# Performance work log

Measured on AMD Instinct MI355X. Metric: run time of the kernel, lower is better.

The kernel has to match this reference:

```python
import jax, jax.numpy as jnp
import numpy as np

N = 50000      # nodes
C = 64         # in_channels
O = 64         # out_channels (== in_channels, required by zeros_like in original)
S = 8          # size: number of weight matrices
E = 1700000    # edges (neighbor pairs incl. self-loops), avg degree ~34


def setup_inputs() -> dict:
    key = jax.random.key(0)
    ks = jax.random.split(key, 9)
    node_tensor = jax.random.normal(ks[0], (N, C), dtype=jnp.float32)
    src = jax.random.randint(ks[1], (E,), 0, N)                 # neighbor node j
    dst = jnp.sort(jax.random.randint(ks[2], (E,), 0, N))       # center node i
    sc = 1.0 / np.sqrt(C)
    W = jax.random.normal(ks[3], (S, C, O), dtype=jnp.float32) * sc   # linears weights
    b = jax.random.normal(ks[4], (S, O), dtype=jnp.float32) * sc      # linears biases
    Ws = jax.random.normal(ks[5], (C, S), dtype=jnp.float32) * sc     # source proj
    bs = jax.random.normal(ks[6], (S,), dtype=jnp.float32) * sc
    Wt = jax.random.normal(ks[7], (C, S), dtype=jnp.float32) * sc     # target proj
    bt = jax.random.normal(ks[8], (S,), dtype=jnp.float32) * sc
    return dict(node_tensor=node_tensor, src=src, dst=dst,
                W=W, b=b, Ws=Ws, bs=bs, Wt=Wt, bt=bt)


def reference(node_tensor, src, dst, W, b, Ws, bs, Wt, bt):
    # Per-node soft-assignment logits (FeaStNet)
    s = node_tensor @ Ws + bs          # [N, S] : source_tensor
    t = node_tensor @ Wt + bt          # [N, S] : target_tensor
    # Per-edge assignment: softmax over the `size` dim of source[center] + target[neighbor]
    q = jax.nn.softmax(s[dst] + t[src], axis=-1)      # [E, S]
    # Per-matrix projected node features: weighted[m] = x @ W_m + b_m
    Wx = jnp.einsum('nc,sco->sno', node_tensor, W) + b[:, None, :]   # [S, N, O]
    # msg[e] = sum_m q[e,m] * Wx[m, src[e]]; loop over small fixed S to avoid [S,E,O] blowup
    msg = q[:, 0:1] * Wx[0][src]                      # [E, O]
    for m in range(1, S):
        msg = msg + q[:, m:m + 1] * Wx[m][src]
    # Scatter-sum over each center's neighborhood, mean over the S weight matrices
    out = jax.ops.segment_sum(msg, dst, num_segments=N) / S          # [N, O]
    return out
```

## Files before the change

### kernel.cpp

```cpp
#include <hip/hip_runtime.h>
#include <hip/hip_bf16.h>


#define CDIM 64
#define SDIM 8

typedef __bf16 bf16x8 __attribute__((ext_vector_type(8)));
typedef float f32x4 __attribute__((ext_vector_type(4)));

__global__ __launch_bounds__(256) void k1_pre(
    const float* __restrict__ x, const float* __restrict__ Ws,
    const float* __restrict__ bs, const float* __restrict__ Wt,
    const float* __restrict__ bt, const float* __restrict__ W,
    const int* __restrict__ dst, float* __restrict__ ST,
    __hip_bfloat16* __restrict__ xbf, __hip_bfloat16* __restrict__ WtB,
    int* __restrict__ rowptr, int N, int E, int nbN) {
  int bid = blockIdx.x;
  if (bid >= nbN + 128) {
    int e = (bid - nbN - 128) * 256 + threadIdx.x;
    if (e >= E) return;
    int a = dst[e];
    int bnd = (e + 1 < E) ? dst[e + 1] : N;
    if (e == 0) {
      for (int d = 0; d <= a; ++d) rowptr[d] = 0;
    }
    for (int d = a + 1; d <= bnd; ++d) rowptr[d] = e + 1;
    return;
  }
  if (bid >= nbN) {
    int t = (bid - nbN) * 256 + threadIdx.x;
    int o = t >> 9, k = t & 511;
    WtB[t] = __float2bfloat16(W[(size_t)k * 64 + o]);
    return;
  }

  __shared__ __hip_bfloat16 wst[16 * 72];
  __shared__ float bst[16];
  int t = threadIdx.x;
#pragma unroll
  for (int j = 0; j < 4; ++j) {
    int idx = t * 4 + j;
    int n = idx >> 6, k = idx & 63;
    float v = (n < 8) ? Ws[k * 8 + n] : Wt[k * 8 + (n - 8)];
    wst[n * 72 + k] = __float2bfloat16(v);
  }
  if (t < 16) bst[t] = (t < 8) ? bs[t] : bt[t - 8];
  __syncthreads();

  int wave = t >> 6, lane = t & 63;
  int r = lane & 15, q = lane >> 4;
  int node = bid * 64 + wave * 16 + r;
  int nodec = node < N ? node : N - 1;
  const float* xr = x + (size_t)nodec * CDIM;

  bf16x8 afrag[2];
#pragma unroll
  for (int kt = 0; kt < 2; ++kt) {
    float4 u0 = *(const float4*)(xr + kt * 32 + q * 8);
    float4 u1 = *(const float4*)(xr + kt * 32 + q * 8 + 4);
    union { bf16x8 v; __hip_bfloat16 h[8]; } a;
    a.h[0] = __float2bfloat16(u0.x); a.h[1] = __float2bfloat16(u0.y);
    a.h[2] = __float2bfloat16(u0.z); a.h[3] = __float2bfloat16(u0.w);
    a.h[4] = __float2bfloat16(u1.x); a.h[5] = __float2bfloat16(u1.y);
    a.h[6] = __float2bfloat16(u1.z); a.h[7] = __float2bfloat16(u1.w);
    afrag[kt] = a.v;
    if (node < N)
      *(bf16x8*)(xbf + (size_t)node * CDIM + kt * 32 + q * 8) = a.v;
  }

  bf16x8 bf0 = *(const bf16x8*)(wst + r * 72 + q * 8);
  bf16x8 bf1 = *(const bf16x8*)(wst + r * 72 + 32 + q * 8);

  f32x4 acc = {0, 0, 0, 0};
  acc = __builtin_amdgcn_mfma_f32_16x16x32_bf16(afrag[0], bf0, acc, 0, 0, 0);
  acc = __builtin_amdgcn_mfma_f32_16x16x32_bf16(afrag[1], bf1, acc, 0, 0, 0);

  int m = lane & 15;
#pragma unroll
  for (int v = 0; v < 4; ++v) {
    int nd = bid * 64 + wave * 16 + q * 4 + v;
    if (nd >= N) continue;
    float val = acc[v] + bst[m];
    if (m >= 8) val = __expf(val);
    ST[nd * 16 + m] = val;
  }
}

__global__ __launch_bounds__(256) void k3_mfma(
    const __hip_bfloat16* __restrict__ xbf, const int* __restrict__ src,
    const int* __restrict__ rowptr, const float* __restrict__ ST,
    __hip_bfloat16* __restrict__ Gbf, float* __restrict__ R, int N) {
  __shared__ __hip_bfloat16 qt_s[4][16 * 40];
  __shared__ __hip_bfloat16 xt_s[4][32 * 72];

  int wave = threadIdx.x >> 6;
  int lane = threadIdx.x & 63;
  int i = blockIdx.x * 4 + wave;
  if (i >= N) return;

  int mm = lane & 7;
  int kk = lane >> 3;
  int mp = lane & 15;
  int q3 = lane >> 4;

  __hip_bfloat16* qt = &qt_s[wave][0];
  __hip_bfloat16* xt = &xt_s[wave][0];

  __hip_bfloat16 z0 = __float2bfloat16(0.0f);
#pragma unroll
  for (int z = 0; z < 5; ++z) qt[320 + z * 64 + lane] = z0;

  int lo = rowptr[i];
  int hi = rowptr[i + 1];
  float uv = __expf(ST[i * 16 + mm]);

  f32x4 acc0 = {0, 0, 0, 0}, acc1 = {0, 0, 0, 0};
  f32x4 acc2 = {0, 0, 0, 0}, acc3 = {0, 0, 0, 0};
  float racc = 0.f;

  if (lo < hi) {
    int ecl = hi - 1;
    int iv[4];
#pragma unroll
    for (int g = 0; g < 4; ++g) {
      int ek = lo + g * 8 + kk;
      iv[g] = src[ek < ecl ? ek : ecl];
    }

    for (int c0 = lo; c0 < hi; c0 += 32) {
      bf16x8 xv[4];
#pragma unroll
      for (int g = 0; g < 4; ++g)
        xv[g] = *(const bf16x8*)(xbf + (size_t)iv[g] * CDIM + mm * 8);

      float tv[4];
#pragma unroll
      for (int g = 0; g < 4; ++g) tv[g] = ST[iv[g] * 16 + 8 + mm];

      int nc0 = c0 + 32;
      int niv[4];
#pragma unroll
      for (int g = 0; g < 4; ++g) {
        int ek = nc0 + g * 8 + kk;
        ek = ek < ecl ? ek : ecl;
        niv[g] = (nc0 < hi) ? src[ek] : iv[g];
      }

#pragma unroll
      for (int g = 0; g < 4; ++g) {
        float w = uv * tv[g];
        float ssum = w + __shfl_xor(w, 1);
        ssum += __shfl_xor(ssum, 2);
        ssum += __shfl_xor(ssum, 4);
        float qv = w * __frcp_rn(ssum);
        if (c0 + g * 8 + kk >= hi) qv = 0.f;
        racc += qv;
        qt[mm * 40 + g * 8 + kk] = __float2bfloat16(qv);
      }

#pragma unroll
      for (int g = 0; g < 4; ++g)
        *(bf16x8*)(xt + (g * 8 + kk) * 72 + mm * 8) = xv[g];

      bf16x8 afrag = *(const bf16x8*)(qt + mp * 40 + q3 * 8);

      {
        union { bf16x8 v; __hip_bfloat16 h[8]; } b0, b1, b2, b3;
#pragma unroll
        for (int j = 0; j < 8; ++j) {
          const __hip_bfloat16* xr = xt + (q3 * 8 + j) * 72 + mp;
          b0.h[j] = xr[0];
          b1.h[j] = xr[16];
          b2.h[j] = xr[32];
          b3.h[j] = xr[48];
        }
        acc0 = __builtin_amdgcn_mfma_f32_16x16x32_bf16(afrag, b0.v, acc0, 0, 0, 0);
        acc1 = __builtin_amdgcn_mfma_f32_16x16x32_bf16(afrag, b1.v, acc1, 0, 0, 0);
        acc2 = __builtin_amdgcn_mfma_f32_16x16x32_bf16(afrag, b2.v, acc2, 0, 0, 0);
        acc3 = __builtin_amdgcn_mfma_f32_16x16x32_bf16(afrag, b3.v, acc3, 0, 0, 0);
      }

      iv[0] = niv[0]; iv[1] = niv[1]; iv[2] = niv[2]; iv[3] = niv[3];
    }
  }

  if (q3 < 2) {
    __hip_bfloat16* Gi = Gbf + (size_t)i * 512;
#pragma unroll
    for (int v = 0; v < 4; ++v) {
      int m = q3 * 4 + v;
      Gi[m * 64 + 0 + mp]  = __float2bfloat16(acc0[v]);
      Gi[m * 64 + 16 + mp] = __float2bfloat16(acc1[v]);
      Gi[m * 64 + 32 + mp] = __float2bfloat16(acc2[v]);
      Gi[m * 64 + 48 + mp] = __float2bfloat16(acc3[v]);
    }
  }

  racc += __shfl_xor(racc, 8);
  racc += __shfl_xor(racc, 16);
  racc += __shfl_xor(racc, 32);
  if (lane < 8) R[(size_t)i * 8 + lane] = racc;
}

__global__ __launch_bounds__(256) void k4_mfma(
    const __hip_bfloat16* __restrict__ Gbf, const float* __restrict__ R,
    const __hip_bfloat16* __restrict__ WtB, const float* __restrict__ bias,
    float* __restrict__ out, int N) {
  __shared__ float4 btile[64 * 65];
  {
    const float4* srcp = (const float4*)WtB;
    int t = threadIdx.x;
#pragma unroll
    for (int j = 0; j < 16; ++j) {
      int ci = t + j * 256;
      btile[(ci >> 6) * 65 + (ci & 63)] = srcp[ci];
    }
  }
  __syncthreads();

  int wave = threadIdx.x >> 6;
  int lane = threadIdx.x & 63;
  int r0 = (blockIdx.x * 4 + wave) * 16;
  if (r0 >= N) return;

  int m = lane & 15;
  int q = lane >> 4;
  const __bf16* abase = (const __bf16*)(Gbf + (size_t)(r0 + m) * 512) + q * 8;
  const __bf16* lbase = (const __bf16*)btile + (size_t)m * 520 + q * 8;

  f32x4 acc0 = {0, 0, 0, 0}, acc1 = {0, 0, 0, 0};
  f32x4 acc2 = {0, 0, 0, 0}, acc3 = {0, 0, 0, 0};
#pragma unroll
  for (int kt = 0; kt < 16; ++kt) {
    bf16x8 a = *(const bf16x8*)(abase + kt * 32);
    bf16x8 b0 = *(const bf16x8*)(lbase + 0 * 520 + kt * 32);
    bf16x8 b1 = *(const bf16x8*)(lbase + 16 * 520 + kt * 32);
    bf16x8 b2 = *(const bf16x8*)(lbase + 32 * 520 + kt * 32);
    bf16x8 b3 = *(const bf16x8*)(lbase + 48 * 520 + kt * 32);
    acc0 = __builtin_amdgcn_mfma_f32_16x16x32_bf16(a, b0, acc0, 0, 0, 0);
    acc1 = __builtin_amdgcn_mfma_f32_16x16x32_bf16(a, b1, acc1, 0, 0, 0);
    acc2 = __builtin_amdgcn_mfma_f32_16x16x32_bf16(a, b2, acc2, 0, 0, 0);
    acc3 = __builtin_amdgcn_mfma_f32_16x16x32_bf16(a, b3, acc3, 0, 0, 0);
  }

#pragma unroll
  for (int v = 0; v < 4; ++v) {
    int ri = r0 + q * 4 + v;
    if (ri >= N) continue;
    const float* Ri = R + (size_t)ri * 8;
    float b0s = 0, b1s = 0, b2s = 0, b3s = 0;
#pragma unroll
    for (int mm = 0; mm < 8; ++mm) {
      float rv = Ri[mm];
      b0s = fmaf(rv, bias[mm * 64 + 0 + m], b0s);
      b1s = fmaf(rv, bias[mm * 64 + 16 + m], b1s);
      b2s = fmaf(rv, bias[mm * 64 + 32 + m], b2s);
      b3s = fmaf(rv, bias[mm * 64 + 48 + m], b3s);
    }
    float* orow = out + (size_t)ri * 64;
    orow[0 + m]  = (acc0[v] + b0s) * 0.125f;
    orow[16 + m] = (acc1[v] + b1s) * 0.125f;
    orow[32 + m] = (acc2[v] + b2s) * 0.125f;
    orow[48 + m] = (acc3[v] + b3s) * 0.125f;
  }
}

extern "C" void kernel_launch(void* const* d_in, const int* in_sizes, int n_in,
                              void* d_out, int out_size, void* d_ws, size_t ws_size,
                              hipStream_t stream) {
  const float* x  = (const float*)d_in[0];
  const int* src  = (const int*)d_in[1];
  const int* dst  = (const int*)d_in[2];
  const float* W  = (const float*)d_in[3];
  const float* b  = (const float*)d_in[4];
  const float* Ws = (const float*)d_in[5];
  const float* bs = (const float*)d_in[6];
  const float* Wt = (const float*)d_in[7];
  const float* bt = (const float*)d_in[8];
  int N = in_sizes[0] / CDIM;
  int E = in_sizes[1];
  float* out = (float*)d_out;

  float* ST = (float*)d_ws;
  __hip_bfloat16* Gbf = (__hip_bfloat16*)(ST + (size_t)N * 16);
  float* R  = (float*)(Gbf + (size_t)N * 512);
  __hip_bfloat16* WtB = (__hip_bfloat16*)(R + (size_t)N * 8);
  __hip_bfloat16* xbf = WtB + 64 * 512;
  int* rowptr = (int*)(xbf + (size_t)N * CDIM);

  int nbN = (N + 63) / 64;
  int nbE = (E + 255) / 256;
  k1_pre<<<nbN + 128 + nbE, 256, 0, stream>>>(x, Ws, bs, Wt, bt, W, dst, ST,
                                              xbf, WtB, rowptr, N, E, nbN);
  k3_mfma<<<(N + 3) / 4, 256, 0, stream>>>(xbf, src, rowptr, ST, Gbf, R, N);
  int mtiles = (N + 15) / 16;
  k4_mfma<<<(mtiles + 3) / 4, 256, 0, stream>>>(Gbf, R, WtB, b, out, N);
}
```

Baseline: 158.3 us.

## Software-pipeline neighbor gathers, use LDS transpose reads, drop k4 weight staging

In the per-node aggregation kernel, the gathers of neighbor features and target logits are now issued one chunk ahead (double buffering), with the source indices prefetched two chunks ahead, so the gather latency can overlap the softmax and MFMA work. The scalar strided LDS reads that built the B fragments are replaced by ds_read_b64_tr_b16 transpose loads over a new 16-wide tiled LDS layout. Launch bounds now request occupancy 4. The final GEMM kernel reads the bf16 weights directly from global memory (cache) instead of staging them in padded LDS with a block barrier. The costs are higher register pressure from the prefetch buffers, inline asm with an explicit full lgkmcnt wait, and weight loads that are no longer served from LDS.

Result: slower. 182.5 us (+15.3%).

```diff
diff --git a/kernel.cpp b/kernel.cpp
--- a/kernel.cpp
+++ b/kernel.cpp
@@ -6,6 +6,7 @@
 #define SDIM 8
 
 typedef __bf16 bf16x8 __attribute__((ext_vector_type(8)));
+typedef __bf16 bf16x4 __attribute__((ext_vector_type(4)));
 typedef float f32x4 __attribute__((ext_vector_type(4)));
 
 __global__ __launch_bounds__(256) void k1_pre(
@@ -86,12 +87,12 @@
   }
 }
 
-__global__ __launch_bounds__(256) void k3_mfma(
+__global__ __launch_bounds__(256, 4) void k3_mfma(
     const __hip_bfloat16* __restrict__ xbf, const int* __restrict__ src,
     const int* __restrict__ rowptr, const float* __restrict__ ST,
     __hip_bfloat16* __restrict__ Gbf, float* __restrict__ R, int N) {
   __shared__ __hip_bfloat16 qt_s[4][16 * 40];
-  __shared__ __hip_bfloat16 xt_s[4][32 * 72];
+  __shared__ __hip_bfloat16 xt_s[4][4 * 32 * 16];
 
   int wave = threadIdx.x >> 6;
   int lane = threadIdx.x & 63;
@@ -114,36 +115,56 @@
   int hi = rowptr[i + 1];
   float uv = __expf(ST[i * 16 + mm]);
 
+  unsigned rd_addr = (unsigned)(uintptr_t)xt + (unsigned)q3 * 256u +
+                     (unsigned)mp * 8u;
+  __hip_bfloat16* xw = xt + (mm >> 1) * 512 + (mm & 1) * 8;
+
   f32x4 acc0 = {0, 0, 0, 0}, acc1 = {0, 0, 0, 0};
   f32x4 acc2 = {0, 0, 0, 0}, acc3 = {0, 0, 0, 0};
   float racc = 0.f;
 
   if (lo < hi) {
     int ecl = hi - 1;
-    int iv[4];
+    int iv[4], niv[4];
+    bf16x8 xv[4];
+    float tv[4];
+
 #pragma unroll
     for (int g = 0; g < 4; ++g) {
       int ek = lo + g * 8 + kk;
       iv[g] = src[ek < ecl ? ek : ecl];
     }
+#pragma unroll
+    for (int g = 0; g < 4; ++g)
+      xv[g] = *(const bf16x8*)(xbf + (size_t)iv[g] * CDIM + mm * 8);
+#pragma unroll
+    for (int g = 0; g < 4; ++g) tv[g] = ST[iv[g] * 16 + 8 + mm];
+    if (lo + 32 < hi) {
+#pragma unroll
+      for (int g = 0; g < 4; ++g) {
+        int ek = lo + 32 + g * 8 + kk;
+        niv[g] = src[ek < ecl ? ek : ecl];
+      }
+    }
 
     for (int c0 = lo; c0 < hi; c0 += 32) {
-      bf16x8 xv[4];
-#pragma unroll
-      for (int g = 0; g < 4; ++g)
-        xv[g] = *(const bf16x8*)(xbf + (size_t)iv[g] * CDIM + mm * 8);
-
-      float tv[4];
-#pragma unroll
-      for (int g = 0; g < 4; ++g) tv[g] = ST[iv[g] * 16 + 8 + mm];
-
-      int nc0 = c0 + 32;
-      int niv[4];
-#pragma unroll
-      for (int g = 0; g < 4; ++g) {
-        int ek = nc0 + g * 8 + kk;
-        ek = ek < ecl ? ek : ecl;
-        niv[g] = (nc0 < hi) ? src[ek] : iv[g];
+      bool hasn = (c0 + 32 < hi);
+      bf16x8 nxv[4];
+      float ntv[4];
+      int nniv[4];
+      if (hasn) {
+#pragma unroll
+        for (int g = 0; g < 4; ++g)
+          nxv[g] = *(const bf16x8*)(xbf + (size_t)niv[g] * CDIM + mm * 8);
+#pragma unroll
+        for (int g = 0; g < 4; ++g) ntv[g] = ST[niv[g] * 16 + 8 + mm];
+        if (c0 + 64 < hi) {
+#pragma unroll
+          for (int g = 0; g < 4; ++g) {
+            int ek = c0 + 64 + g * 8 + kk;
+            nniv[g] = src[ek < ecl ? ek : ecl];
+          }
+        }
       }
 
 #pragma unroll
@@ -160,27 +181,47 @@
 
 #pragma unroll
       for (int g = 0; g < 4; ++g)
-        *(bf16x8*)(xt + (g * 8 + kk) * 72 + mm * 8) = xv[g];
+        *(bf16x8*)(xw + (g * 8 + kk) * 16) = xv[g];
 
       bf16x8 afrag = *(const bf16x8*)(qt + mp * 40 + q3 * 8);
 
-      {
-        union { bf16x8 v; __hip_bfloat16 h[8]; } b0, b1, b2, b3;
-#pragma unroll
-        for (int j = 0; j < 8; ++j) {
-          const __hip_bfloat16* xr = xt + (q3 * 8 + j) * 72 + mp;
-          b0.h[j] = xr[0];
-          b1.h[j] = xr[16];
-          b2.h[j] = xr[32];
-          b3.h[j] = xr[48];
+      bf16x4 t0, t1, t2, t3, t4, t5, t6, t7;
+      asm volatile(
+          "ds_read_b64_tr_b16 %0, %8 offset:0\n\t"
+          "ds_read_b64_tr_b16 %1, %8 offset:128\n\t"
+          "ds_read_b64_tr_b16 %2, %8 offset:1024\n\t"
+          "ds_read_b64_tr_b16 %3, %8 offset:1152\n\t"
+          "ds_read_b64_tr_b16 %4, %8 offset:2048\n\t"
+          "ds_read_b64_tr_b16 %5, %8 offset:2176\n\t"
+          "ds_read_b64_tr_b16 %6, %8 offset:3072\n\t"
+          "ds_read_b64_tr_b16 %7, %8 offset:3200"
+          : "=&v"(t0), "=&v"(t1), "=&v"(t2), "=&v"(t3),
+            "=&v"(t4), "=&v"(t5), "=&v"(t6), "=&v"(t7)
+          : "v"(rd_addr)
+          : "memory");
+      asm volatile("s_waitcnt lgkmcnt(0)" ::: "memory");
+      __builtin_amdgcn_sched_barrier(0);
+
+      union { bf16x8 v; bf16x4 h[2]; } b0, b1, b2, b3;
+      b0.h[0] = t0; b0.h[1] = t1;
+      b1.h[0] = t2; b1.h[1] = t3;
+      b2.h[0] = t4; b2.h[1] = t5;
+      b3.h[0] = t6; b3.h[1] = t7;
+
+      acc0 = __builtin_amdgcn_mfma_f32_16x16x32_bf16(afrag, b0.v, acc0, 0, 0, 0);
+      acc1 = __builtin_amdgcn_mfma_f32_16x16x32_bf16(afrag, b1.v, acc1, 0, 0, 0);
+      acc2 = __builtin_amdgcn_mfma_f32_16x16x32_bf16(afrag, b2.v, acc2, 0, 0, 0);
+      acc3 = __builtin_amdgcn_mfma_f32_16x16x32_bf16(afrag, b3.v, acc3, 0, 0, 0);
+
+      if (hasn) {
+#pragma unroll
+        for (int g = 0; g < 4; ++g) {
+          iv[g] = niv[g];
+          xv[g] = nxv[g];
+          tv[g] = ntv[g];
+          niv[g] = nniv[g];
         }
-        acc0 = __builtin_amdgcn_mfma_f32_16x16x32_bf16(afrag, b0.v, acc0, 0, 0, 0);
-        acc1 = __builtin_amdgcn_mfma_f32_16x16x32_bf16(afrag, b1.v, acc1, 0, 0, 0);
-        acc2 = __builtin_amdgcn_mfma_f32_16x16x32_bf16(afrag, b2.v, acc2, 0, 0, 0);
-        acc3 = __builtin_amdgcn_mfma_f32_16x16x32_bf16(afrag, b3.v, acc3, 0, 0, 0);
       }
-
-      iv[0] = niv[0]; iv[1] = niv[1]; iv[2] = niv[2]; iv[3] = niv[3];
     }
   }
 
@@ -206,18 +247,6 @@
     const __hip_bfloat16* __restrict__ Gbf, const float* __restrict__ R,
     const __hip_bfloat16* __restrict__ WtB, const float* __restrict__ bias,
     float* __restrict__ out, int N) {
-  __shared__ float4 btile[64 * 65];
-  {
-    const float4* srcp = (const float4*)WtB;
-    int t = threadIdx.x;
-#pragma unroll
-    for (int j = 0; j < 16; ++j) {
-      int ci = t + j * 256;
-      btile[(ci >> 6) * 65 + (ci & 63)] = srcp[ci];
-    }
-  }
-  __syncthreads();
-
   int wave = threadIdx.x >> 6;
   int lane = threadIdx.x & 63;
   int r0 = (blockIdx.x * 4 + wave) * 16;
@@ -226,17 +255,17 @@
   int m = lane & 15;
   int q = lane >> 4;
   const __bf16* abase = (const __bf16*)(Gbf + (size_t)(r0 + m) * 512) + q * 8;
-  const __bf16* lbase = (const __bf16*)btile + (size_t)m * 520 + q * 8;
+  const __bf16* wbase = (const __bf16*)WtB + (size_t)m * 512 + q * 8;
 
   f32x4 acc0 = {0, 0, 0, 0}, acc1 = {0, 0, 0, 0};
   f32x4 acc2 = {0, 0, 0, 0}, acc3 = {0, 0, 0, 0};
 #pragma unroll
   for (int kt = 0; kt < 16; ++kt) {
     bf16x8 a = *(const bf16x8*)(abase + kt * 32);
-    bf16x8 b0 = *(const bf16x8*)(lbase + 0 * 520 + kt * 32);
-    bf16x8 b1 = *(const bf16x8*)(lbase + 16 * 520 + kt * 32);
-    bf16x8 b2 = *(const bf16x8*)(lbase + 32 * 520 + kt * 32);
-    bf16x8 b3 = *(const bf16x8*)(lbase + 48 * 520 + kt * 32);
+    bf16x8 b0 = *(const bf16x8*)(wbase + 0 * 8192 + kt * 32);
+    bf16x8 b1 = *(const bf16x8*)(wbase + 1 * 8192 + kt * 32);
+    bf16x8 b2 = *(const bf16x8*)(wbase + 2 * 8192 + kt * 32);
+    bf16x8 b3 = *(const bf16x8*)(wbase + 3 * 8192 + kt * 32);
     acc0 = __builtin_amdgcn_mfma_f32_16x16x32_bf16(a, b0, acc0, 0, 0, 0);
     acc1 = __builtin_amdgcn_mfma_f32_16x16x32_bf16(a, b1, acc1, 0, 0, 0);
     acc2 = __builtin_amdgcn_mfma_f32_16x16x32_bf16(a, b2, acc2, 0, 0, 0);
```
